# Kernel optimization log

Hardware: AMD Instinct MI355X
Metric: run time of the kernel (lower is better)

The kernel has to match this reference:

```python
import jax, jax.numpy as jnp
import numpy as np

B, L, H, NHEADS = 32, 1024, 128, 2
HEAD = H // NHEADS
NEG = -2.0**32 + 1.0  # padding value used by the torch module


def setup_inputs() -> dict:
    key = jax.random.key(0)
    ks = jax.random.split(key, 9)
    queries = jax.random.normal(ks[0], (B, L, H), dtype=jnp.float32)
    keys = jax.random.normal(ks[1], (B, L, H), dtype=jnp.float32)
    time_mask = jax.random.bernoulli(ks[2], 0.1, (B, L))
    # causal mask: True above the diagonal (future positions masked)
    attn_mask = jnp.triu(jnp.ones((L, L), dtype=bool), k=1)
    s = 1.0 / np.sqrt(H)
    Qw = jax.random.uniform(ks[3], (H, H), jnp.float32, -s, s)
    Qb = jax.random.uniform(ks[4], (H,), jnp.float32, -s, s)
    Kw = jax.random.uniform(ks[5], (H, H), jnp.float32, -s, s)
    Kb = jax.random.uniform(ks[6], (H,), jnp.float32, -s, s)
    Vw = jax.random.uniform(ks[7], (H, H), jnp.float32, -s, s)
    Vb = jax.random.uniform(ks[8], (H,), jnp.float32, -s, s)
    return {"queries": queries, "keys": keys, "time_mask": time_mask,
            "attn_mask": attn_mask, "Qw": Qw, "Qb": Qb, "Kw": Kw, "Kb": Kb,
            "Vw": Vw, "Vb": Vb}


def reference(queries, keys, time_mask, attn_mask, Qw, Qb, Kw, Kb, Vw, Vb):
    b, l, h = queries.shape
    d = h // NHEADS
    # torch Linear: x @ W.T + b
    Q = queries @ Qw.T + Qb
    K = keys @ Kw.T + Kb
    V = keys @ Vw.T + Vb
    # split heads: torch cat(split(dim=2), dim=0) == (h, B, L, d) layout;
    # equivalent per-head math with (B, h, L, d):
    Qh = Q.reshape(b, l, NHEADS, d).transpose(0, 2, 1, 3)  # bhld
    Kh = K.reshape(b, l, NHEADS, d).transpose(0, 2, 1, 3)
    Vh = V.reshape(b, l, NHEADS, d).transpose(0, 2, 1, 3)
    scores = jnp.einsum('bhqd,bhkd->bhqk', Qh, Kh) / jnp.sqrt(
        jnp.asarray(d, dtype=Qh.dtype))
    # time_mask masks whole query rows; attn_mask is causal over (q, k)
    scores = jnp.where(time_mask[:, None, :, None], NEG, scores)
    scores = jnp.where(attn_mask[None, None, :, :], NEG, scores)
    attn = jax.nn.softmax(scores, axis=-1)  # dropout_rate=0 -> identity
    out = jnp.einsum('bhqk,bhkd->bhqd', attn, Vh)
    return out.transpose(0, 2, 1, 3).reshape(b, l, h)
```

## Files before the change

### kernel.cpp

```cpp
#include <hip/hip_runtime.h>

#define LSEQ 1024
#define DH 64
#define NH 2

typedef __attribute__((ext_vector_type(8))) __bf16 bf16x8;
typedef __attribute__((ext_vector_type(4))) float f32x4;
typedef __attribute__((ext_vector_type(16))) float f32x16;
typedef __attribute__((ext_vector_type(4))) unsigned u32x4;
typedef __attribute__((ext_vector_type(8))) unsigned short ushort8;

__device__ __forceinline__ unsigned short f2bf(float f) {
  unsigned u = __float_as_uint(f);
  u += 0x7FFFu + ((u >> 16) & 1u);
  return (unsigned short)(u >> 16);
}
__device__ __forceinline__ unsigned cvt_pk_bf16(float lo, float hi) {
  unsigned r;
  asm("v_cvt_pk_bf16_f32 %0, %1, %2" : "=v"(r) : "v"(lo), "v"(hi));
  return r;
}
__device__ __forceinline__ void gload16(const void* g, void* l) {
  __builtin_amdgcn_global_load_lds(
      (const __attribute__((address_space(1))) void*)g,
      (__attribute__((address_space(3))) void*)l, 16, 0, 0);
}

#define QSCALE 0.1803368801111601f

__global__ __launch_bounds__(256) void wconv_kernel(
    const float* __restrict__ Qw, const float* __restrict__ Kw,
    const float* __restrict__ Vw, unsigned short* __restrict__ Wbf,
    float* __restrict__ Vmean)
{
  const int t = blockIdx.x * 256 + threadIdx.x;
  if (t < NH * 32 * DH) Vmean[t] = 0.f;
  const int m = t >> 12;
  const float* W = (m == 0) ? Qw : (m == 1) ? Kw : Vw;
  const float4 v = ((const float4*)W)[t & 4095];
  uint2 u;
  u.x = cvt_pk_bf16(v.x, v.y);
  u.y = cvt_pk_bf16(v.z, v.w);
  *(uint2*)&Wbf[t * 4] = u;
}

__global__ __launch_bounds__(256, 2) void proj_kernel(
    const float* __restrict__ queries, const float* __restrict__ keys,
    const unsigned short* __restrict__ Wbf,
    const float* __restrict__ Qb, const float* __restrict__ Kb,
    const float* __restrict__ Vb,
    unsigned short* __restrict__ Qbf, unsigned short* __restrict__ Kbf,
    unsigned short* __restrict__ Vt, float* __restrict__ Vmean)
{
  constexpr int LP = 136;
  __shared__ __align__(16) unsigned short Xs[128 * LP];
  __shared__ __align__(16) unsigned short Ws[16384];

  const int t = threadIdx.x;
  const int lane = t & 63, w = t >> 6;
  const int c = lane & 15, g = lane >> 4;
  const int wrow = w * 32;

  const int mat = blockIdx.x & 1;
  const int rt  = (blockIdx.x >> 1) * 128;
  const float* Xin = mat ? keys : queries;

#define WSTAGE(wi) do {                                                    \
    const char* Wg_ = (const char*)(Wbf + (wi) * 16384);                   \
    _Pragma("unroll")                                                      \
    for (int i_ = 0; i_ < 8; ++i_) {                                       \
      const int off_ = t * 16 + i_ * 4096;                                 \
      const int sch_ = ((((off_ >> 4) & 15) ^ ((off_ >> 8) & 7)) << 4);    \
      gload16(Wg_ + (off_ & ~0xFF) + sch_,                                 \
              (char*)Ws + w * 1024 + i_ * 4096);                           \
    }                                                                      \
  } while (0)

#define WFRAG(ct_, kc_) \
  (*(const bf16x8*)&Ws[((ct_) * 16 + c) * 128 + ((((kc_) * 4 + g) ^ (c & 7)) << 3)])

#define XFRAG(half_, kc_) \
  (*(const bf16x8*)&Xs[(wrow + (half_) * 16 + c) * LP + (kc_) * 32 + g * 8])

  WSTAGE(mat);

  const float4* X4 = (const float4*)(Xin + (size_t)rt * 128);
#pragma unroll
  for (int i = 0; i < 16; ++i) {
    const int e4 = t + i * 256;
    const float4 v = X4[e4];
    const int e = e4 * 4;
    uint2 u;
    u.x = cvt_pk_bf16(v.x, v.y);
    u.y = cvt_pk_bf16(v.z, v.w);
    *(uint2*)&Xs[(e >> 7) * LP + (e & 127)] = u;
  }
  __syncthreads();

  f32x4 accA[2][8];
#pragma unroll
  for (int i = 0; i < 2; ++i)
#pragma unroll
    for (int j = 0; j < 8; ++j) accA[i][j] = (f32x4){0.f, 0.f, 0.f, 0.f};

#pragma unroll
  for (int kc = 0; kc < 4; ++kc) {
    const bf16x8 a0 = XFRAG(0, kc);
    const bf16x8 a1 = XFRAG(1, kc);
#pragma unroll
    for (int ct = 0; ct < 8; ++ct) {
      const bf16x8 bfr = WFRAG(ct, kc);
      accA[0][ct] = __builtin_amdgcn_mfma_f32_16x16x32_bf16(a0, bfr, accA[0][ct], 0, 0, 0);
      accA[1][ct] = __builtin_amdgcn_mfma_f32_16x16x32_bf16(a1, bfr, accA[1][ct], 0, 0, 0);
    }
  }

  f32x4 accB[2][8];
  if (mat) {
    __syncthreads();
    WSTAGE(2);
    __syncthreads();

#pragma unroll
    for (int i = 0; i < 2; ++i)
#pragma unroll
      for (int j = 0; j < 8; ++j) accB[i][j] = (f32x4){0.f, 0.f, 0.f, 0.f};

#pragma unroll
    for (int kc = 0; kc < 4; ++kc) {
      const bf16x8 a0 = XFRAG(0, kc);
      const bf16x8 a1 = XFRAG(1, kc);
#pragma unroll
      for (int ct = 0; ct < 8; ++ct) {
        const bf16x8 bfr = WFRAG(ct, kc);
        accB[0][ct] = __builtin_amdgcn_mfma_f32_16x16x32_bf16(a0, bfr, accB[0][ct], 0, 0, 0);
        accB[1][ct] = __builtin_amdgcn_mfma_f32_16x16x32_bf16(a1, bfr, accB[1][ct], 0, 0, 0);
      }
    }

#pragma unroll
    for (int ct = 0; ct < 8; ++ct) {
      const float bv = Vb[ct * 16 + c];
      float cs = 8.f * bv;
#pragma unroll
      for (int qf = 0; qf < 2; ++qf)
#pragma unroll
        for (int r = 0; r < 4; ++r) cs += accB[qf][ct][r];
      cs += __shfl_xor(cs, 16);
      cs += __shfl_xor(cs, 32);
      if (g == 0) {
        const int col = ct * 16 + c;
        const int bh = (rt >> 10) * NH + (col >> 6);
        atomicAdd(&Vmean[bh * DH + (col & 63)], cs);
      }
    }
  }

  __syncthreads();
  {
    const float* biasA = mat ? Kb : Qb;
    const float qs = mat ? 1.0f : QSCALE;
#pragma unroll
    for (int qf = 0; qf < 2; ++qf)
#pragma unroll
      for (int ct = 0; ct < 8; ++ct) {
        const float bv = biasA[ct * 16 + c];
#pragma unroll
        for (int r = 0; r < 4; ++r)
          Xs[(wrow + qf * 16 + g * 4 + r) * LP + ct * 16 + c] =
              f2bf((accA[qf][ct][r] + bv) * qs);
      }
  }
  __syncthreads();
  {
    unsigned short* outp = (mat ? Kbf : Qbf) + (size_t)rt * 128;
#pragma unroll
    for (int i = 0; i < 8; ++i) {
      const int e = i * 2048 + t * 8;
      *(ushort8*)&outp[e] = *(const ushort8*)&Xs[(e >> 7) * LP + (e & 127)];
    }
  }

  if (mat) {
    __syncthreads();
#pragma unroll
    for (int qf = 0; qf < 2; ++qf)
#pragma unroll
      for (int ct = 0; ct < 8; ++ct) {
        const float bv = Vb[ct * 16 + c];
        const int col = ct * 16 + c;
        uint2 u;
        u.x = cvt_pk_bf16(accB[qf][ct][0] + bv, accB[qf][ct][1] + bv);
        u.y = cvt_pk_bf16(accB[qf][ct][2] + bv, accB[qf][ct][3] + bv);
        *(uint2*)&Xs[col * LP + wrow + qf * 16 + g * 4] = u;
      }
    __syncthreads();
    const int b = rt >> 10, l0 = rt & 1023;
#pragma unroll
    for (int i = 0; i < 8; ++i) {
      const int e = i * 2048 + t * 8;
      const int col = e >> 7, li = e & 127;
      const ushort8 v8 = *(const ushort8*)&Xs[col * LP + li];
      const int hh = col >> 6, dh = col & 63;
      unsigned short* vp = Vt + ((size_t)(b * NH + hh)) * (DH * LSEQ) +
                           (size_t)dh * LSEQ + l0 + li;
      *(ushort8*)vp = v8;
    }
  }
#undef WSTAGE
#undef WFRAG
#undef XFRAG
}

__global__ __launch_bounds__(128, 2) void attn_kernel(
    const unsigned short* __restrict__ Qbf, const unsigned short* __restrict__ Kbf,
    const unsigned short* __restrict__ Vt, const float* __restrict__ Vmean,
    const int* __restrict__ time_mask, float* __restrict__ out)
{
  __shared__ __align__(16) char smem[33280];

  const int tid = threadIdx.x;
  const int lane = tid & 63, w = tid >> 6;
  const int lq = lane & 31, hi = lane >> 5;
  const int s7 = lq & 7;

  const int wgid = blockIdx.x;
  const int xcd = wgid & 7;
  const int idx = wgid >> 3;
  const int bh  = xcd * 8 + (idx & 7);
  const int qt  = 15 - (idx >> 3);
  const int qbase = qt * 64;
  const int b = bh >> 1, h = bh & 1;

  const unsigned short* Qp = Qbf + ((size_t)b * LSEQ) * 128 + h * 64;
  const char* Kpb = (const char*)(Kbf + ((size_t)b * LSEQ) * 128 + h * 64);
  const char* Vpb = (const char*)(Vt + (size_t)bh * (DH * LSEQ));

  const int nkv = qt + 1;

#define STAGE(tkv, bi) do {                                                   \
    const int kv_ = (tkv) * 64;                                               \
    _Pragma("unroll")                                                         \
    for (int r_ = 0; r_ < 4; ++r_) {                                          \
      const int off_ = tid * 16 + r_ * 2048;                                  \
      const int row_ = off_ >> 7;                                             \
      const int chk_ = (((off_ >> 4) & 7) ^ (row_ & 7)) << 4;                 \
      gload16(Kpb + (size_t)(kv_ + row_) * 256 + chk_,                        \
              (char*)smem + (bi) * 8192 + r_ * 2048 + tid * 16);              \
      gload16(Vpb + (size_t)row_ * 2048 + kv_ * 2 + chk_,                     \
              (char*)smem + 16384 + (bi) * 8192 + r_ * 2048 + tid * 16);      \
    }                                                                         \
  } while (0)

#define PLSWAP(x_, y_) asm("v_permlane32_swap_b32 %0, %1" : "+v"(x_), "+v"(y_))

#define MKPA(pk_, m_, dst_) do {                                              \
    unsigned x0_ = pk_[4*(m_)], x1_ = pk_[4*(m_)+1];                          \
    unsigned y0_ = pk_[4*(m_)+2], y1_ = pk_[4*(m_)+3];                        \
    PLSWAP(x0_, y0_); PLSWAP(x1_, y1_);                                       \
    u32x4 u_ = {x0_, x1_, y0_, y1_};                                          \
    dst_ = *(bf16x8*)&u_;                                                     \
  } while (0)

  bf16x8 qa[4];
#pragma unroll
  for (int kc4 = 0; kc4 < 4; ++kc4)
    qa[kc4] = *(const bf16x8*)&Qp[(qbase + w * 32 + lq) * 128 + kc4 * 16 + hi * 8];

  const __bf16 one = (__bf16)1.0f;
  const bf16x8 vones = {one, one, one, one, one, one, one, one};

  f32x16 acc0 = {}, acc1 = {}, acc5 = {};

  STAGE(0, 0);
  __syncthreads();

  for (int tk = 0; tk < nkv; ++tk) {
    const int cur = tk & 1;
    if (tk + 1 < nkv) STAGE(tk + 1, cur ^ 1);

    const char* Kl = smem + cur * 8192;
    const char* Vl = smem + 16384 + cur * 8192;

    f32x16 s0 = {}, s1 = {};
    __builtin_amdgcn_s_setprio(1);
#pragma unroll
    for (int kc4 = 0; kc4 < 4; ++kc4) {
      const bf16x8 kf = *(const bf16x8*)(Kl + (lq << 7) + (((2 * kc4 + hi) ^ s7) << 4));
      s0 = __builtin_amdgcn_mfma_f32_32x32x16_bf16(kf, qa[kc4], s0, 0, 0, 0);
    }
#pragma unroll
    for (int kc4 = 0; kc4 < 4; ++kc4) {
      const bf16x8 kf = *(const bf16x8*)(Kl + ((32 + lq) << 7) + (((2 * kc4 + hi) ^ s7) << 4));
      s1 = __builtin_amdgcn_mfma_f32_32x32x16_bf16(kf, qa[kc4], s1, 0, 0, 0);
    }
    __builtin_amdgcn_s_setprio(0);

    bf16x8 vf[4][2];
#pragma unroll
    for (int kc4 = 0; kc4 < 4; ++kc4)
#pragma unroll
      for (int dt = 0; dt < 2; ++dt)
        vf[kc4][dt] = *(const bf16x8*)(Vl + ((dt * 32 + lq) << 7) + (((2 * kc4 + hi) ^ s7) << 4));

    const bool diag = (tk == nkv - 1);
    const int kv = tk * 64;
    const int qrow = qbase + w * 32 + lq;
    float p0[16], p1[16];
#pragma unroll
    for (int r = 0; r < 16; ++r) {
      const int krow = (r & 3) + 8 * (r >> 2) + 4 * hi;
      float e0 = __builtin_amdgcn_exp2f(s0[r]);
      float e1 = __builtin_amdgcn_exp2f(s1[r]);
      if (diag) {
        if (kv + krow > qrow)      e0 = 0.f;
        if (kv + 32 + krow > qrow) e1 = 0.f;
      }
      p0[r] = e0; p1[r] = e1;
    }

    unsigned pk0[8], pk1[8];
#pragma unroll
    for (int bb = 0; bb < 4; ++bb) {
      pk0[2*bb]   = cvt_pk_bf16(p0[4*bb],   p0[4*bb+1]);
      pk0[2*bb+1] = cvt_pk_bf16(p0[4*bb+2], p0[4*bb+3]);
      pk1[2*bb]   = cvt_pk_bf16(p1[4*bb],   p1[4*bb+1]);
      pk1[2*bb+1] = cvt_pk_bf16(p1[4*bb+2], p1[4*bb+3]);
    }

    bf16x8 pa;
    __builtin_amdgcn_s_setprio(1);
    MKPA(pk0, 0, pa);
    acc0 = __builtin_amdgcn_mfma_f32_32x32x16_bf16(pa, vf[0][0], acc0, 0, 0, 0);
    acc1 = __builtin_amdgcn_mfma_f32_32x32x16_bf16(pa, vf[0][1], acc1, 0, 0, 0);
    acc5 = __builtin_amdgcn_mfma_f32_32x32x16_bf16(pa, vones,    acc5, 0, 0, 0);
    MKPA(pk0, 1, pa);
    acc0 = __builtin_amdgcn_mfma_f32_32x32x16_bf16(pa, vf[1][0], acc0, 0, 0, 0);
    acc1 = __builtin_amdgcn_mfma_f32_32x32x16_bf16(pa, vf[1][1], acc1, 0, 0, 0);
    acc5 = __builtin_amdgcn_mfma_f32_32x32x16_bf16(pa, vones,    acc5, 0, 0, 0);
    MKPA(pk1, 0, pa);
    acc0 = __builtin_amdgcn_mfma_f32_32x32x16_bf16(pa, vf[2][0], acc0, 0, 0, 0);
    acc1 = __builtin_amdgcn_mfma_f32_32x32x16_bf16(pa, vf[2][1], acc1, 0, 0, 0);
    acc5 = __builtin_amdgcn_mfma_f32_32x32x16_bf16(pa, vones,    acc5, 0, 0, 0);
    MKPA(pk1, 1, pa);
    acc0 = __builtin_amdgcn_mfma_f32_32x32x16_bf16(pa, vf[3][0], acc0, 0, 0, 0);
    acc1 = __builtin_amdgcn_mfma_f32_32x32x16_bf16(pa, vf[3][1], acc1, 0, 0, 0);
    acc5 = __builtin_amdgcn_mfma_f32_32x32x16_bf16(pa, vones,    acc5, 0, 0, 0);
    __builtin_amdgcn_s_setprio(0);

    __syncthreads();
  }

  int* tmx = (int*)(smem + 32768 + w * 128);
  if (hi == 0)
    tmx[lq] = time_mask[b * LSEQ + qbase + w * 32 + lq];
  asm volatile("s_waitcnt lgkmcnt(0)" ::: "memory");
  __builtin_amdgcn_sched_barrier(0);

  const float vmv0 = Vmean[bh * DH + lq]      * (1.0f / 1024.0f);
  const float vmv1 = Vmean[bh * DH + 32 + lq] * (1.0f / 1024.0f);

#pragma unroll
  for (int r = 0; r < 16; ++r) {
    const int qr = (r & 3) + 8 * (r >> 2) + 4 * hi;
    const int tm = tmx[qr];
    const float wv = 1.0f / acc5[r];
    float* orow = out + (size_t)(b * LSEQ + qbase + w * 32 + qr) * (NH * DH) + h * DH;
    orow[lq]      = tm ? vmv0 : acc0[r] * wv;
    orow[32 + lq] = tm ? vmv1 : acc1[r] * wv;
  }
#undef STAGE
#undef PLSWAP
#undef MKPA
}

extern "C" void kernel_launch(void* const* d_in, const int* in_sizes, int n_in,
                              void* d_out, int out_size, void* d_ws, size_t ws_size,
                              hipStream_t stream) {
  const float* queries   = (const float*)d_in[0];
  const float* keys      = (const float*)d_in[1];
  const int*   time_mask = (const int*)d_in[2];
  const float* Qw = (const float*)d_in[4];
  const float* Qb = (const float*)d_in[5];
  const float* Kw = (const float*)d_in[6];
  const float* Kb = (const float*)d_in[7];
  const float* Vw = (const float*)d_in[8];
  const float* Vb = (const float*)d_in[9];
  float* out = (float*)d_out;

  char* ws = (char*)d_ws;
  unsigned short* Wbf   = (unsigned short*)(ws);
  float*          Vmean = (float*)(ws + 98304);
  unsigned short* Qbf   = (unsigned short*)(ws + 114688);
  unsigned short* Kbf   = (unsigned short*)(ws + 8503296);
  unsigned short* Vtp   = (unsigned short*)(ws + 16891904);

  wconv_kernel<<<48, 256, 0, stream>>>(Qw, Kw, Vw, Wbf, Vmean);
  proj_kernel<<<512, 256, 0, stream>>>(queries, keys, Wbf, Qb, Kb, Vb,
                                       Qbf, Kbf, Vtp, Vmean);
  attn_kernel<<<1024, 128, 0, stream>>>(Qbf, Kbf, Vtp, Vmean, time_mask, out);
}
```

Baseline: 47.97 us.

## Single-buffer V, compute row sums in registers, raise occupancy to three blocks

The attention kernel now keeps only one V buffer and double-buffers K alone, which cuts shared memory and allows three workgroups per CU via launch bounds. V for the current tile and K for the next are issued together, then a partial vmcnt wait and a barrier follow. The row-sum MFMA against a ones vector is replaced by a scalar fp32 accumulation of the exponentials plus a permlane swap reduction. The time mask is folded into an inverse-sum value stored in LDS. The V load is no longer prefetched a full iteration ahead, so its latency is exposed at each step. The row sum now uses the unrounded fp32 values rather than the bf16 ones fed to the MFMA, and the extra dummy K load on the last iteration adds a little traffic.

New measurement: 49.71 us. +3.6%, slower.

```diff
diff --git a/kernel.cpp b/kernel.cpp
--- a/kernel.cpp
+++ b/kernel.cpp
@@ -212,12 +212,12 @@
 #undef XFRAG
 }
 
-__global__ __launch_bounds__(128, 2) void attn_kernel(
+__global__ __launch_bounds__(128, 3) void attn_kernel(
     const unsigned short* __restrict__ Qbf, const unsigned short* __restrict__ Kbf,
     const unsigned short* __restrict__ Vt, const float* __restrict__ Vmean,
     const int* __restrict__ time_mask, float* __restrict__ out)
 {
-  __shared__ __align__(16) char smem[33280];
+  __shared__ __align__(16) char smem[24832];
 
   const int tid = threadIdx.x;
   const int lane = tid & 63, w = tid >> 6;
@@ -238,7 +238,7 @@
 
   const int nkv = qt + 1;
 
-#define STAGE(tkv, bi) do {                                                   \
+#define STAGE_K(tkv, bi) do {                                                 \
     const int kv_ = (tkv) * 64;                                               \
     _Pragma("unroll")                                                         \
     for (int r_ = 0; r_ < 4; ++r_) {                                          \
@@ -246,9 +246,19 @@
       const int row_ = off_ >> 7;                                             \
       const int chk_ = (((off_ >> 4) & 7) ^ (row_ & 7)) << 4;                 \
       gload16(Kpb + (size_t)(kv_ + row_) * 256 + chk_,                        \
-              (char*)smem + (bi) * 8192 + r_ * 2048 + tid * 16);              \
+              (char*)smem + (bi) * 8192 + off_);                              \
+    }                                                                         \
+  } while (0)
+
+#define STAGE_V(tkv) do {                                                     \
+    const int kv_ = (tkv) * 64;                                               \
+    _Pragma("unroll")                                                         \
+    for (int r_ = 0; r_ < 4; ++r_) {                                          \
+      const int off_ = tid * 16 + r_ * 2048;                                  \
+      const int row_ = off_ >> 7;                                             \
+      const int chk_ = (((off_ >> 4) & 7) ^ (row_ & 7)) << 4;                 \
       gload16(Vpb + (size_t)row_ * 2048 + kv_ * 2 + chk_,                     \
-              (char*)smem + 16384 + (bi) * 8192 + r_ * 2048 + tid * 16);      \
+              (char*)smem + 16384 + off_);                                    \
     }                                                                         \
   } while (0)
 
@@ -267,20 +277,21 @@
   for (int kc4 = 0; kc4 < 4; ++kc4)
     qa[kc4] = *(const bf16x8*)&Qp[(qbase + w * 32 + lq) * 128 + kc4 * 16 + hi * 8];
 
-  const __bf16 one = (__bf16)1.0f;
-  const bf16x8 vones = {one, one, one, one, one, one, one, one};
-
-  f32x16 acc0 = {}, acc1 = {}, acc5 = {};
-
-  STAGE(0, 0);
-  __syncthreads();
+  f32x16 acc0 = {}, acc1 = {};
+  float lsum = 0.f;
+
+  STAGE_K(0, 0);
 
   for (int tk = 0; tk < nkv; ++tk) {
-    const int cur = tk & 1;
-    if (tk + 1 < nkv) STAGE(tk + 1, cur ^ 1);
-
-    const char* Kl = smem + cur * 8192;
-    const char* Vl = smem + 16384 + cur * 8192;
+    STAGE_V(tk);
+    if (tk + 1 < nkv) STAGE_K(tk + 1, (tk + 1) & 1);
+    else              STAGE_K(tk, (tk + 1) & 1);
+    asm volatile("s_waitcnt vmcnt(4)" ::: "memory");
+    __builtin_amdgcn_s_barrier();
+    __builtin_amdgcn_sched_barrier(0);
+
+    const char* Kl = smem + (tk & 1) * 8192;
+    const char* Vl = smem + 16384;
 
     f32x16 s0 = {}, s1 = {};
     __builtin_amdgcn_s_setprio(1);
@@ -296,80 +307,88 @@
     }
     __builtin_amdgcn_s_setprio(0);
 
-    bf16x8 vf[4][2];
-#pragma unroll
-    for (int kc4 = 0; kc4 < 4; ++kc4)
-#pragma unroll
-      for (int dt = 0; dt < 2; ++dt)
-        vf[kc4][dt] = *(const bf16x8*)(Vl + ((dt * 32 + lq) << 7) + (((2 * kc4 + hi) ^ s7) << 4));
-
     const bool diag = (tk == nkv - 1);
     const int kv = tk * 64;
     const int qrow = qbase + w * 32 + lq;
-    float p0[16], p1[16];
-#pragma unroll
-    for (int r = 0; r < 16; ++r) {
-      const int krow = (r & 3) + 8 * (r >> 2) + 4 * hi;
-      float e0 = __builtin_amdgcn_exp2f(s0[r]);
-      float e1 = __builtin_amdgcn_exp2f(s1[r]);
-      if (diag) {
-        if (kv + krow > qrow)      e0 = 0.f;
-        if (kv + 32 + krow > qrow) e1 = 0.f;
+
+    unsigned pk0[8], pk1[8];
+#pragma unroll
+    for (int bb = 0; bb < 4; ++bb) {
+      float e[4], f[4];
+#pragma unroll
+      for (int j = 0; j < 4; ++j) {
+        const int r = 4 * bb + j;
+        const int krow = (r & 3) + 8 * (r >> 2) + 4 * hi;
+        e[j] = __builtin_amdgcn_exp2f(s0[r]);
+        f[j] = __builtin_amdgcn_exp2f(s1[r]);
+        if (diag) {
+          if (kv + krow > qrow)      e[j] = 0.f;
+          if (kv + 32 + krow > qrow) f[j] = 0.f;
+        }
+        lsum += e[j] + f[j];
       }
-      p0[r] = e0; p1[r] = e1;
-    }
-
-    unsigned pk0[8], pk1[8];
-#pragma unroll
-    for (int bb = 0; bb < 4; ++bb) {
-      pk0[2*bb]   = cvt_pk_bf16(p0[4*bb],   p0[4*bb+1]);
-      pk0[2*bb+1] = cvt_pk_bf16(p0[4*bb+2], p0[4*bb+3]);
-      pk1[2*bb]   = cvt_pk_bf16(p1[4*bb],   p1[4*bb+1]);
-      pk1[2*bb+1] = cvt_pk_bf16(p1[4*bb+2], p1[4*bb+3]);
-    }
+      pk0[2*bb]   = cvt_pk_bf16(e[0], e[1]);
+      pk0[2*bb+1] = cvt_pk_bf16(e[2], e[3]);
+      pk1[2*bb]   = cvt_pk_bf16(f[0], f[1]);
+      pk1[2*bb+1] = cvt_pk_bf16(f[2], f[3]);
+    }
+
+    bf16x8 vf[4][2];
+#pragma unroll
+    for (int kc4 = 0; kc4 < 4; ++kc4)
+#pragma unroll
+      for (int dt = 0; dt < 2; ++dt)
+        vf[kc4][dt] = *(const bf16x8*)(Vl + ((dt * 32 + lq) << 7) + (((2 * kc4 + hi) ^ s7) << 4));
 
     bf16x8 pa;
     __builtin_amdgcn_s_setprio(1);
     MKPA(pk0, 0, pa);
     acc0 = __builtin_amdgcn_mfma_f32_32x32x16_bf16(pa, vf[0][0], acc0, 0, 0, 0);
     acc1 = __builtin_amdgcn_mfma_f32_32x32x16_bf16(pa, vf[0][1], acc1, 0, 0, 0);
-    acc5 = __builtin_amdgcn_mfma_f32_32x32x16_bf16(pa, vones,    acc5, 0, 0, 0);
     MKPA(pk0, 1, pa);
     acc0 = __builtin_amdgcn_mfma_f32_32x32x16_bf16(pa, vf[1][0], acc0, 0, 0, 0);
     acc1 = __builtin_amdgcn_mfma_f32_32x32x16_bf16(pa, vf[1][1], acc1, 0, 0, 0);
-    acc5 = __builtin_amdgcn_mfma_f32_32x32x16_bf16(pa, vones,    acc5, 0, 0, 0);
     MKPA(pk1, 0, pa);
     acc0 = __builtin_amdgcn_mfma_f32_32x32x16_bf16(pa, vf[2][0], acc0, 0, 0, 0);
     acc1 = __builtin_amdgcn_mfma_f32_32x32x16_bf16(pa, vf[2][1], acc1, 0, 0, 0);
-    acc5 = __builtin_amdgcn_mfma_f32_32x32x16_bf16(pa, vones,    acc5, 0, 0, 0);
     MKPA(pk1, 1, pa);
     acc0 = __builtin_amdgcn_mfma_f32_32x32x16_bf16(pa, vf[3][0], acc0, 0, 0, 0);
     acc1 = __builtin_amdgcn_mfma_f32_32x32x16_bf16(pa, vf[3][1], acc1, 0, 0, 0);
-    acc5 = __builtin_amdgcn_mfma_f32_32x32x16_bf16(pa, vones,    acc5, 0, 0, 0);
     __builtin_amdgcn_s_setprio(0);
 
-    __syncthreads();
-  }
-
-  int* tmx = (int*)(smem + 32768 + w * 128);
-  if (hi == 0)
-    tmx[lq] = time_mask[b * LSEQ + qbase + w * 32 + lq];
+    __builtin_amdgcn_s_barrier();
+  }
+
+  float pa_ = lsum, pb_ = lsum;
+  PLSWAP(pa_, pb_);
+  const float total = lsum + (hi ? pa_ : pb_);
+
+  float* lsx = (float*)(smem + 24576 + w * 128);
+  if (hi == 0) {
+    const int tm = time_mask[b * LSEQ + qbase + w * 32 + lq];
+    lsx[lq] = tm ? -1.0f : 1.0f / total;
+  }
   asm volatile("s_waitcnt lgkmcnt(0)" ::: "memory");
   __builtin_amdgcn_sched_barrier(0);
 
+  f32x4 inv4[4];
+#pragma unroll
+  for (int bb = 0; bb < 4; ++bb)
+    inv4[bb] = *(const f32x4*)&lsx[8 * bb + 4 * hi];
+
   const float vmv0 = Vmean[bh * DH + lq]      * (1.0f / 1024.0f);
   const float vmv1 = Vmean[bh * DH + 32 + lq] * (1.0f / 1024.0f);
 
 #pragma unroll
   for (int r = 0; r < 16; ++r) {
     const int qr = (r & 3) + 8 * (r >> 2) + 4 * hi;
-    const int tm = tmx[qr];
-    const float wv = 1.0f / acc5[r];
+    const float wv = inv4[r >> 2][r & 3];
     float* orow = out + (size_t)(b * LSEQ + qbase + w * 32 + qr) * (NH * DH) + h * DH;
-    orow[lq]      = tm ? vmv0 : acc0[r] * wv;
-    orow[32 + lq] = tm ? vmv1 : acc1[r] * wv;
-  }
-#undef STAGE
+    orow[lq]      = (wv < 0.f) ? vmv0 : acc0[r] * wv;
+    orow[32 + lq] = (wv < 0.f) ? vmv1 : acc1[r] * wv;
+  }
+#undef STAGE_K
+#undef STAGE_V
 #undef PLSWAP
 #undef MKPA
 }
```

## Split projection into one block per weight matrix with half-size weight staging

Applied to the files above, without the earlier changes.

The projection kernel now launches 768 blocks, each computing a single one of Q, K or V for a 128-row tile, instead of 512 blocks where key blocks computed both K and V. Weight staging in LDS is halved by loading the K dimension in two halves, which cuts shared memory per block and allows a launch bound of three blocks per CU. This removes the load imbalance between query and key blocks and raises occupancy. The cost is that the keys tile is loaded and converted twice, and there is an extra barrier-separated weight reload in the middle of the K loop.

After: 46.29 us (median of 2 runs). 3.5% less time.

```diff
diff --git a/kernel.cpp b/kernel.cpp
--- a/kernel.cpp
+++ b/kernel.cpp
@@ -44,7 +44,7 @@
   *(uint2*)&Wbf[t * 4] = u;
 }
 
-__global__ __launch_bounds__(256, 2) void proj_kernel(
+__global__ __launch_bounds__(256, 3) void proj_kernel(
     const float* __restrict__ queries, const float* __restrict__ keys,
     const unsigned short* __restrict__ Wbf,
     const float* __restrict__ Qb, const float* __restrict__ Kb,
@@ -54,35 +54,36 @@
 {
   constexpr int LP = 136;
   __shared__ __align__(16) unsigned short Xs[128 * LP];
-  __shared__ __align__(16) unsigned short Ws[16384];
+  __shared__ __align__(16) unsigned short Wh[8192];
 
   const int t = threadIdx.x;
   const int lane = t & 63, w = t >> 6;
   const int c = lane & 15, g = lane >> 4;
   const int wrow = w * 32;
 
-  const int mat = blockIdx.x & 1;
-  const int rt  = (blockIdx.x >> 1) * 128;
-  const float* Xin = mat ? keys : queries;
-
-#define WSTAGE(wi) do {                                                    \
-    const char* Wg_ = (const char*)(Wbf + (wi) * 16384);                   \
+  const int mat = blockIdx.x >> 8;
+  const int rt  = (blockIdx.x & 255) * 128;
+  const float* Xin = (mat == 0) ? queries : keys;
+  const char* Wg = (const char*)(Wbf + mat * 16384);
+
+#define WSTAGE_H(h) do {                                                   \
     _Pragma("unroll")                                                      \
-    for (int i_ = 0; i_ < 8; ++i_) {                                       \
-      const int off_ = t * 16 + i_ * 4096;                                 \
-      const int sch_ = ((((off_ >> 4) & 15) ^ ((off_ >> 8) & 7)) << 4);    \
-      gload16(Wg_ + (off_ & ~0xFF) + sch_,                                 \
-              (char*)Ws + w * 1024 + i_ * 4096);                           \
+    for (int i_ = 0; i_ < 4; ++i_) {                                       \
+      const int off_ = t * 16 + i_ * 4096;                   \
+      const int lrow_ = off_ >> 7;                             \
+      const int lch_ = (off_ >> 4) & 7;                                    \
+      gload16(Wg + lrow_ * 256 + (h) * 128 + ((lch_ ^ (lrow_ & 7)) << 4),  \
+              (char*)Wh + off_);                                           \
     }                                                                      \
   } while (0)
 
-#define WFRAG(ct_, kc_) \
-  (*(const bf16x8*)&Ws[((ct_) * 16 + c) * 128 + ((((kc_) * 4 + g) ^ (c & 7)) << 3)])
+#define WFRAG_H(ct_, j_) \
+  (*(const bf16x8*)&Wh[((ct_) * 16 + c) * 64 + (((j_) ^ (c & 7)) << 3)])
 
 #define XFRAG(half_, kc_) \
   (*(const bf16x8*)&Xs[(wrow + (half_) * 16 + c) * LP + (kc_) * 32 + g * 8])
 
-  WSTAGE(mat);
+  WSTAGE_H(0);
 
   const float4* X4 = (const float4*)(Xin + (size_t)rt * 128);
 #pragma unroll
@@ -97,47 +98,40 @@
   }
   __syncthreads();
 
-  f32x4 accA[2][8];
+  f32x4 acc[2][8];
 #pragma unroll
   for (int i = 0; i < 2; ++i)
 #pragma unroll
-    for (int j = 0; j < 8; ++j) accA[i][j] = (f32x4){0.f, 0.f, 0.f, 0.f};
-
-#pragma unroll
-  for (int kc = 0; kc < 4; ++kc) {
-    const bf16x8 a0 = XFRAG(0, kc);
-    const bf16x8 a1 = XFRAG(1, kc);
+    for (int j = 0; j < 8; ++j) acc[i][j] = (f32x4){0.f, 0.f, 0.f, 0.f};
+
+#pragma unroll
+  for (int kc2 = 0; kc2 < 2; ++kc2) {
+    const bf16x8 a0 = XFRAG(0, kc2);
+    const bf16x8 a1 = XFRAG(1, kc2);
 #pragma unroll
     for (int ct = 0; ct < 8; ++ct) {
-      const bf16x8 bfr = WFRAG(ct, kc);
-      accA[0][ct] = __builtin_amdgcn_mfma_f32_16x16x32_bf16(a0, bfr, accA[0][ct], 0, 0, 0);
-      accA[1][ct] = __builtin_amdgcn_mfma_f32_16x16x32_bf16(a1, bfr, accA[1][ct], 0, 0, 0);
-    }
-  }
-
-  f32x4 accB[2][8];
-  if (mat) {
-    __syncthreads();
-    WSTAGE(2);
-    __syncthreads();
-
-#pragma unroll
-    for (int i = 0; i < 2; ++i)
-#pragma unroll
-      for (int j = 0; j < 8; ++j) accB[i][j] = (f32x4){0.f, 0.f, 0.f, 0.f};
-
-#pragma unroll
-    for (int kc = 0; kc < 4; ++kc) {
-      const bf16x8 a0 = XFRAG(0, kc);
-      const bf16x8 a1 = XFRAG(1, kc);
-#pragma unroll
-      for (int ct = 0; ct < 8; ++ct) {
-        const bf16x8 bfr = WFRAG(ct, kc);
-        accB[0][ct] = __builtin_amdgcn_mfma_f32_16x16x32_bf16(a0, bfr, accB[0][ct], 0, 0, 0);
-        accB[1][ct] = __builtin_amdgcn_mfma_f32_16x16x32_bf16(a1, bfr, accB[1][ct], 0, 0, 0);
-      }
-    }
-
+      const bf16x8 bfr = WFRAG_H(ct, kc2 * 4 + g);
+      acc[0][ct] = __builtin_amdgcn_mfma_f32_16x16x32_bf16(a0, bfr, acc[0][ct], 0, 0, 0);
+      acc[1][ct] = __builtin_amdgcn_mfma_f32_16x16x32_bf16(a1, bfr, acc[1][ct], 0, 0, 0);
+    }
+  }
+  __syncthreads();
+  WSTAGE_H(1);
+  __syncthreads();
+
+#pragma unroll
+  for (int kc2 = 0; kc2 < 2; ++kc2) {
+    const bf16x8 a0 = XFRAG(0, kc2 + 2);
+    const bf16x8 a1 = XFRAG(1, kc2 + 2);
+#pragma unroll
+    for (int ct = 0; ct < 8; ++ct) {
+      const bf16x8 bfr = WFRAG_H(ct, kc2 * 4 + g);
+      acc[0][ct] = __builtin_amdgcn_mfma_f32_16x16x32_bf16(a0, bfr, acc[0][ct], 0, 0, 0);
+      acc[1][ct] = __builtin_amdgcn_mfma_f32_16x16x32_bf16(a1, bfr, acc[1][ct], 0, 0, 0);
+    }
+  }
+
+  if (mat == 2) {
 #pragma unroll
     for (int ct = 0; ct < 8; ++ct) {
       const float bv = Vb[ct * 16 + c];
@@ -145,7 +139,7 @@
 #pragma unroll
       for (int qf = 0; qf < 2; ++qf)
 #pragma unroll
-        for (int r = 0; r < 4; ++r) cs += accB[qf][ct][r];
+        for (int r = 0; r < 4; ++r) cs += acc[qf][ct][r];
       cs += __shfl_xor(cs, 16);
       cs += __shfl_xor(cs, 32);
       if (g == 0) {
@@ -154,34 +148,6 @@
         atomicAdd(&Vmean[bh * DH + (col & 63)], cs);
       }
     }
-  }
-
-  __syncthreads();
-  {
-    const float* biasA = mat ? Kb : Qb;
-    const float qs = mat ? 1.0f : QSCALE;
-#pragma unroll
-    for (int qf = 0; qf < 2; ++qf)
-#pragma unroll
-      for (int ct = 0; ct < 8; ++ct) {
-        const float bv = biasA[ct * 16 + c];
-#pragma unroll
-        for (int r = 0; r < 4; ++r)
-          Xs[(wrow + qf * 16 + g * 4 + r) * LP + ct * 16 + c] =
-              f2bf((accA[qf][ct][r] + bv) * qs);
-      }
-  }
-  __syncthreads();
-  {
-    unsigned short* outp = (mat ? Kbf : Qbf) + (size_t)rt * 128;
-#pragma unroll
-    for (int i = 0; i < 8; ++i) {
-      const int e = i * 2048 + t * 8;
-      *(ushort8*)&outp[e] = *(const ushort8*)&Xs[(e >> 7) * LP + (e & 127)];
-    }
-  }
-
-  if (mat) {
     __syncthreads();
 #pragma unroll
     for (int qf = 0; qf < 2; ++qf)
@@ -190,8 +156,8 @@
         const float bv = Vb[ct * 16 + c];
         const int col = ct * 16 + c;
         uint2 u;
-        u.x = cvt_pk_bf16(accB[qf][ct][0] + bv, accB[qf][ct][1] + bv);
-        u.y = cvt_pk_bf16(accB[qf][ct][2] + bv, accB[qf][ct][3] + bv);
+        u.x = cvt_pk_bf16(acc[qf][ct][0] + bv, acc[qf][ct][1] + bv);
+        u.y = cvt_pk_bf16(acc[qf][ct][2] + bv, acc[qf][ct][3] + bv);
         *(uint2*)&Xs[col * LP + wrow + qf * 16 + g * 4] = u;
       }
     __syncthreads();
@@ -206,9 +172,30 @@
                            (size_t)dh * LSEQ + l0 + li;
       *(ushort8*)vp = v8;
     }
-  }
-#undef WSTAGE
-#undef WFRAG
+  } else {
+    const float* biasA = mat ? Kb : Qb;
+    const float qs = mat ? 1.0f : QSCALE;
+    __syncthreads();
+#pragma unroll
+    for (int qf = 0; qf < 2; ++qf)
+#pragma unroll
+      for (int ct = 0; ct < 8; ++ct) {
+        const float bv = biasA[ct * 16 + c];
+#pragma unroll
+        for (int r = 0; r < 4; ++r)
+          Xs[(wrow + qf * 16 + g * 4 + r) * LP + ct * 16 + c] =
+              f2bf((acc[qf][ct][r] + bv) * qs);
+      }
+    __syncthreads();
+    unsigned short* outp = (mat ? Kbf : Qbf) + (size_t)rt * 128;
+#pragma unroll
+    for (int i = 0; i < 8; ++i) {
+      const int e = i * 2048 + t * 8;
+      *(ushort8*)&outp[e] = *(const ushort8*)&Xs[(e >> 7) * LP + (e & 127)];
+    }
+  }
+#undef WSTAGE_H
+#undef WFRAG_H
 #undef XFRAG
 }
 
@@ -396,7 +383,7 @@
   unsigned short* Vtp   = (unsigned short*)(ws + 16891904);
 
   wconv_kernel<<<48, 256, 0, stream>>>(Qw, Kw, Vw, Wbf, Vmean);
-  proj_kernel<<<512, 256, 0, stream>>>(queries, keys, Wbf, Qb, Kb, Vb,
+  proj_kernel<<<768, 256, 0, stream>>>(queries, keys, Wbf, Qb, Kb, Vb,
                                        Qbf, Kbf, Vtp, Vmean);
   attn_kernel<<<1024, 128, 0, stream>>>(Qbf, Kbf, Vtp, Vmean, time_mask, out);
 }
```
